# Optimization experiments

Measured on AMD Instinct MI355X. Metric: run time of the kernel, lower is better.

The kernel has to match this reference:

```python
import jax, jax.numpy as jnp
import numpy as np
import math

DIM = 4096
N_HEADS = 32
HEAD_DIM = DIM // N_HEADS  # 128
SEQLEN = 2048


def setup_inputs() -> dict:
    key = jax.random.key(0)
    ks = jax.random.split(key, 8)
    x = jax.random.normal(ks[0], (1, SEQLEN, DIM), dtype=jnp.float32)
    # freqs_cis as real view: (seqlen, head_dim//2, 2) = (cos, sin) of rotary angles
    theta = 10000.0 ** (-jnp.arange(0, HEAD_DIM, 2, dtype=jnp.float32) / HEAD_DIM)
    angles = jnp.arange(SEQLEN, dtype=jnp.float32)[:, None] * theta[None, :]
    freqs = jnp.stack([jnp.cos(angles), jnp.sin(angles)], axis=-1)  # (S, 64, 2)
    # causal additive mask (use -1e9 instead of -inf for numeric safety)
    mask = jnp.triu(jnp.full((SEQLEN, SEQLEN), -1e9, dtype=jnp.float32), k=1)[None, None]
    scale = 1.0 / math.sqrt(DIM)
    wq = jax.random.normal(ks[1], (DIM, DIM), dtype=jnp.float32) * scale
    wk = jax.random.normal(ks[2], (DIM, DIM), dtype=jnp.float32) * scale
    wv = jax.random.normal(ks[3], (DIM, DIM), dtype=jnp.float32) * scale
    wo = jax.random.normal(ks[4], (DIM, DIM), dtype=jnp.float32) * scale
    return {"x": x, "start_pos": 0, "freqs": freqs, "mask": mask,
            "wq": wq, "wk": wk, "wv": wv, "wo": wo}


def _rotary(xq, xk, freqs, seqlen, n_heads, head_dim):
    # Faithful to source: note the repo's slice(0, 2) means xq_ == xq (no pair swap).
    ll = freqs[:, :, 0:1]  # (S, hd/2, 1) cos
    rr = freqs[:, :, 1:2]  # (S, hd/2, 1) sin
    fl = jnp.concatenate([ll, ll], axis=-1).reshape(seqlen, 1, head_dim)
    fr = jnp.concatenate([-rr, rr], axis=-1).reshape(seqlen, 1, head_dim)
    xq_ = xq.reshape(seqlen, n_heads, head_dim // 2, 2).reshape(seqlen, n_heads, head_dim)  # == xq
    xk_ = xk.reshape(seqlen, n_heads, head_dim // 2, 2).reshape(seqlen, n_heads, head_dim)  # == xk
    return xq * fl + xq_ * fr, xk * fl + xk_ * fr


def reference(x, start_pos, freqs, mask, wq, wk, wv, wo):
    bsz, seqlen, dim = x.shape  # bsz == 1 (source squeezes batch)
    xs = x[0]  # (S, D) -- HE encrypt/linear/decrypt roundtrip == plain linear
    xq = xs @ wq.T
    xk = xs @ wk.T
    xv = xs @ wv.T
    xq = xq.reshape(seqlen, N_HEADS, HEAD_DIM)
    xk = xk.reshape(seqlen, N_HEADS, HEAD_DIM)
    xv = xv.reshape(seqlen, N_HEADS, HEAD_DIM)
    xq, xk = _rotary(xq, xk, freqs, seqlen, N_HEADS, HEAD_DIM)
    # start_pos == 0 and zero-initialized cache => keys/values are just xk/xv
    q = jnp.transpose(xq, (1, 0, 2))  # (H, S, Dh)
    k = jnp.transpose(xk, (1, 0, 2))
    v = jnp.transpose(xv, (1, 0, 2))
    scores = jnp.einsum('hqd,hkd->hqk', q, k) / math.sqrt(HEAD_DIM)  # (H, S, S)
    scores = scores[None] + mask  # (1, H, S, S)
    probs = jax.nn.softmax(scores, axis=-1)
    out = jnp.einsum('bhqk,hkd->bhqd', probs, v)  # (1, H, S, Dh)
    out = jnp.transpose(out, (0, 2, 1, 3)).reshape(bsz, seqlen, dim)
    return out @ wo.T
```

## Files before the change

kernel.cpp:

```cpp
#include <hip/hip_runtime.h>

#define DIM 4096
#define SEQ 2048
#define NH 32
#define HD 128

typedef __bf16 bf16x8 __attribute__((ext_vector_type(8)));
typedef float f32x4 __attribute__((ext_vector_type(4)));

#define QSCALE 0.12751649736765598f

__device__ inline ushort f2bf(float f) {
    union { float f; unsigned u; } v; v.f = f;
    unsigned r = v.u + 0x7fffu + ((v.u >> 16) & 1u);
    return (ushort)(r >> 16);
}

__global__ void conv_all(const float* __restrict__ x,  const float* __restrict__ wq,
                         const float* __restrict__ wk, const float* __restrict__ wv,
                         const float* __restrict__ wo,
                         ushort* __restrict__ xb,  ushort* __restrict__ wqb,
                         ushort* __restrict__ wkb, ushort* __restrict__ wvb,
                         ushort* __restrict__ wob) {
    int i = blockIdx.x * 256 + threadIdx.x;
    const float* src; ushort* dst; int off;
    const int n4x = (SEQ * DIM) / 4;
    if (i < n4x) { src = x; dst = xb; off = i; }
    else {
        int j = i - n4x;
        int w = j >> 22;
        off = j & ((1 << 22) - 1);
        src = (w == 0) ? wq : (w == 1) ? wk : (w == 2) ? wv : wo;
        dst = (w == 0) ? wqb : (w == 1) ? wkb : (w == 2) ? wvb : wob;
    }
    float4 v = ((const float4*)src)[off];
    ushort4 o;
    o.x = f2bf(v.x); o.y = f2bf(v.y); o.z = f2bf(v.z); o.w = f2bf(v.w);
    ((ushort4*)dst)[off] = o;
}


#define AS1(p) (const __attribute__((address_space(1))) void*)(p)
#define AS3(p) (__attribute__((address_space(3))) void*)(p)
#define FENCE() asm volatile("" ::: "memory")
#define BARRIER() do { FENCE(); __builtin_amdgcn_sched_barrier(0); \
    __builtin_amdgcn_s_barrier(); \
    __builtin_amdgcn_sched_barrier(0); FENCE(); } while (0)
#define LGKM0() do { asm volatile("s_waitcnt lgkmcnt(0)" ::: "memory"); \
    __builtin_amdgcn_sched_barrier(0); } while (0)

__device__ __forceinline__ void gemm256_body(
    const ushort* __restrict__ Ab,
    const ushort* __restrict__ Bb,
    ushort* __restrict__ sA0, ushort* __restrict__ sA1,
    ushort* __restrict__ sB0, ushort* __restrict__ sB1,
    f32x4 acc[8][4], const int K)
{
    const int tid  = threadIdx.x;
    const int wave = tid >> 6, lane = tid & 63;
    const int quad = lane >> 4, c = lane & 15;
    const int wm = wave >> 2, wn = wave & 3;

    const int aoff = (lane >> 3) * K + (((lane & 7) ^ (lane >> 3)) * 8);
    const int sa_r0 = wave * 8;
    const int sb_r0 = (wave >> 1) * 64 + (wave & 1) * 16;

    const int rp0 = ((0 * 4 + quad) ^ (c & 7)) * 8;
    const int rp1 = ((1 * 4 + quad) ^ (c & 7)) * 8;
    const int arow = (wm * 128 + c) * 64;
    const int brow = (wn * 64 + c) * 64;

#define STAGE_A(dst, h, k0) do { \
    const int _r0 = (h) * 64 + sa_r0; \
    __builtin_amdgcn_global_load_lds(AS1(Ab + (size_t)_r0 * K + (k0) + aoff), \
                                     AS3((dst) + _r0 * 64), 16, 0, 0); \
    const int _r1 = _r0 + 128; \
    __builtin_amdgcn_global_load_lds(AS1(Ab + (size_t)_r1 * K + (k0) + aoff), \
                                     AS3((dst) + _r1 * 64), 16, 0, 0); \
  } while (0)
#define STAGE_B(dst, h, k0) do { \
    const int _r0 = (h) * 32 + sb_r0; \
    __builtin_amdgcn_global_load_lds(AS1(Bb + (size_t)_r0 * K + (k0) + aoff), \
                                     AS3((dst) + _r0 * 64), 16, 0, 0); \
    const int _r1 = _r0 + 8; \
    __builtin_amdgcn_global_load_lds(AS1(Bb + (size_t)_r1 * K + (k0) + aoff), \
                                     AS3((dst) + _r1 * 64), 16, 0, 0); \
  } while (0)

    bf16x8 af[4][2], bfr[2][2];

#define READ_AH(buf, mh) do { \
    _Pragma("unroll") \
    for (int mt = 0; mt < 4; ++mt) { \
        af[mt][0] = *(const bf16x8*)&(buf)[arow + (mh) * 4096 + mt * 1024 + rp0]; \
        af[mt][1] = *(const bf16x8*)&(buf)[arow + (mh) * 4096 + mt * 1024 + rp1]; \
    } } while (0)
#define READ_BH(buf, nh) do { \
    _Pragma("unroll") \
    for (int nt = 0; nt < 2; ++nt) { \
        bfr[nt][0] = *(const bf16x8*)&(buf)[brow + (nh) * 2048 + nt * 1024 + rp0]; \
        bfr[nt][1] = *(const bf16x8*)&(buf)[brow + (nh) * 2048 + nt * 1024 + rp1]; \
    } } while (0)
#define MMA_Q(mh, nh) do { \
    __builtin_amdgcn_s_setprio(1); \
    _Pragma("unroll") \
    for (int kk = 0; kk < 2; ++kk) \
    _Pragma("unroll") \
    for (int mt = 0; mt < 4; ++mt) \
    _Pragma("unroll") \
    for (int nt = 0; nt < 2; ++nt) \
        acc[(mh)*4+mt][(nh)*2+nt] = __builtin_amdgcn_mfma_f32_16x16x32_bf16( \
            af[mt][kk], bfr[nt][kk], acc[(mh)*4+mt][(nh)*2+nt], 0, 0, 0); \
    __builtin_amdgcn_s_setprio(0); \
  } while (0)

    const int NT = K >> 6;

    STAGE_A(sA0, 0, 0);  STAGE_B(sB0, 0, 0);
    STAGE_A(sA0, 1, 0);  STAGE_B(sB0, 1, 0);
    STAGE_A(sA1, 0, 64); STAGE_B(sB1, 0, 64);
    asm volatile("s_waitcnt vmcnt(4)" ::: "memory");
    BARRIER();

    for (int t = 0; t < NT; ++t) {
        ushort* cA = (t & 1) ? sA1 : sA0;
        ushort* cB = (t & 1) ? sB1 : sB0;
        ushort* nA = (t & 1) ? sA0 : sA1;
        ushort* nB = (t & 1) ? sB0 : sB1;
        const int kn  = (t + 1) << 6;
        const int kn2 = (t + 2) << 6;
        const bool ok1 = (t + 1 < NT), ok2 = (t + 2 < NT);

        READ_AH(cA, 0); READ_BH(cB, 0);
        if (ok1) STAGE_A(nA, 1, kn);
        BARRIER(); LGKM0();
        MMA_Q(0, 0);
        BARRIER();

        READ_BH(cB, 1);
        if (ok1) STAGE_B(nB, 1, kn);
        BARRIER(); LGKM0();
        MMA_Q(0, 1);
        BARRIER();

        READ_AH(cA, 1); READ_BH(cB, 0);
        if (ok2) STAGE_A(cA, 0, kn2);
        BARRIER(); LGKM0();
        MMA_Q(1, 0);
        BARRIER();

        READ_BH(cB, 1);
        if (ok2) STAGE_B(cB, 0, kn2);
        BARRIER(); LGKM0();
        MMA_Q(1, 1);
        if (t < NT - 1) {
            if (ok2) asm volatile("s_waitcnt vmcnt(4)" ::: "memory");
            else     asm volatile("s_waitcnt vmcnt(0)" ::: "memory");
        }
        BARRIER();
    }
#undef STAGE_A
#undef STAGE_B
#undef READ_AH
#undef READ_BH
#undef MMA_Q
}

__global__ __launch_bounds__(512, 2)
void gemm_qkv(const ushort* __restrict__ A,
              const ushort* __restrict__ Bq, const ushort* __restrict__ Bk,
              const ushort* __restrict__ Bv,
              ushort* __restrict__ qout, ushort* __restrict__ kout,
              ushort* __restrict__ vt, const float* __restrict__ freqs) {
    __shared__ __align__(16) ushort sA[2][256 * 64];
    __shared__ __align__(16) ushort sB[2][256 * 64];
    const int bi = blockIdx.x;
    const int x = bi & 7;
    const int l = bi >> 3;
    const int mblk = l & 7;
    const int nblk = x * 6 + (l >> 3);
    const int wsel = nblk >> 4;
    const int nloc = (nblk & 15) * 256;
    const int m0 = mblk * 256;
    const ushort* B = (wsel == 0) ? Bq : (wsel == 1) ? Bk : Bv;

    const f32x4 vzero = {0.f, 0.f, 0.f, 0.f};
    f32x4 acc[8][4];
#pragma unroll
    for (int i = 0; i < 8; i++)
#pragma unroll
        for (int j = 0; j < 4; j++) acc[i][j] = vzero;

    gemm256_body(A + (size_t)m0 * DIM, B + (size_t)nloc * DIM,
                 &sA[0][0], &sA[1][0], &sB[0][0], &sB[1][0], acc, DIM);

    const int tid = threadIdx.x;
    const int wave = tid >> 6, lane = tid & 63;
    const int quad = lane >> 4, c = lane & 15;
    const int wm = wave >> 2, wn = wave & 3;

    if (wsel < 2) {
        ushort* Cw = wsel ? kout : qout;
        const float qs = wsel ? 1.0f : QSCALE;
#pragma unroll
        for (int i = 0; i < 8; i++) {
#pragma unroll
            for (int j = 0; j < 4; j++) {
                int colg = nloc + wn * 64 + j * 16 + c;
                int dh = (colg & 127) >> 1;
#pragma unroll
                for (int r = 0; r < 4; r++) {
                    int row = m0 + wm * 128 + i * 16 + quad * 4 + r;
                    float2 f2 = ((const float2*)freqs)[row * 64 + dh];
                    float f = (f2.x + ((c & 1) ? f2.y : -f2.y)) * qs;
                    Cw[(size_t)row * DIM + colg] = f2bf(acc[i][j][r] * f);
                }
            }
        }
    } else {
#pragma unroll
        for (int i = 0; i < 8; i++) {
#pragma unroll
            for (int j = 0; j < 4; j++) {
                int cv = nloc + wn * 64 + j * 16 + c;
                int row0 = m0 + wm * 128 + i * 16 + quad * 4;
                ushort4 o;
                o.x = f2bf(acc[i][j][0]); o.y = f2bf(acc[i][j][1]);
                o.z = f2bf(acc[i][j][2]); o.w = f2bf(acc[i][j][3]);
                *(ushort4*)&vt[(size_t)cv * SEQ + row0] = o;
            }
        }
    }
}

__global__ __launch_bounds__(512, 2)
void gemm_f32out(const ushort* __restrict__ A, const ushort* __restrict__ B,
                 float* __restrict__ C, int M, int N, int K) {
    __shared__ __align__(16) ushort sA[2][256 * 64];
    __shared__ __align__(16) ushort sB[2][256 * 64];
    const int bi = blockIdx.x;
    const int x = bi & 7;
    const int l = bi >> 3;
    const int mblk = l & 7;
    const int nblk = x * 2 + (l >> 3);
    const int m0 = mblk * 256, n0 = nblk * 256;

    const f32x4 vzero = {0.f, 0.f, 0.f, 0.f};
    f32x4 acc[8][4];
#pragma unroll
    for (int i = 0; i < 8; i++)
#pragma unroll
        for (int j = 0; j < 4; j++) acc[i][j] = vzero;

    gemm256_body(A + (size_t)m0 * K, B + (size_t)n0 * K,
                 &sA[0][0], &sA[1][0], &sB[0][0], &sB[1][0], acc, K);

    const int tid = threadIdx.x;
    const int wave = tid >> 6, lane = tid & 63;
    const int quad = lane >> 4, c = lane & 15;
    const int wm = wave >> 2, wn = wave & 3;

#pragma unroll
    for (int i = 0; i < 8; i++)
#pragma unroll
        for (int j = 0; j < 4; j++)
#pragma unroll
            for (int r = 0; r < 4; r++) {
                int row = m0 + wm * 128 + i * 16 + quad * 4 + r;
                int col = n0 + wn * 64 + j * 16 + c;
                C[(size_t)row * N + col] = acc[i][j][r];
            }
}

__global__ __launch_bounds__(256)
void flash_kernel(const ushort* __restrict__ Q, const ushort* __restrict__ K,
                  const ushort* __restrict__ Vt, ushort* __restrict__ O) {
    const int bi = blockIdx.x;
    const int h = bi & (NH - 1);
    const int p = bi >> 5;
    __shared__ __align__(16) ushort sK[64 * 128];
    __shared__ __align__(16) ushort sVt[128 * 64];
    __shared__ __align__(16) ushort sP[4][16 * 72];
    const int tid = threadIdx.x, wave = tid >> 6, lane = tid & 63;
    const int quad = lane >> 4, c = lane & 15;

    for (int pass = 0; pass < 2; pass++) {
        const int qb = pass ? (SEQ / 64 - 1 - p) : p;
        const int q0 = qb * 64;

        bf16x8 qf[4];
        {
            const ushort* Qp = Q + (size_t)(q0 + wave * 16 + c) * DIM + h * HD;
#pragma unroll
            for (int ks = 0; ks < 4; ks++) qf[ks] = *(const bf16x8*)(Qp + ks * 32 + quad * 8);
        }
        const f32x4 vzero = {0.f, 0.f, 0.f, 0.f};
        f32x4 oa[8];
#pragma unroll
        for (int dt = 0; dt < 8; dt++) oa[dt] = vzero;
        float ms[4], ls[4];
#pragma unroll
        for (int r = 0; r < 4; r++) { ms[r] = -1e30f; ls[r] = 0.f; }

        for (int kt = 0; kt <= qb; kt++) {
            __syncthreads();
#pragma unroll
            for (int i = 0; i < 4; i++) {
                int lr = wave * 16 + i * 4 + (lane >> 4);
                int ch = lane & 15;
                int g = (ch & 8) | ((ch ^ lr) & 7);
                __builtin_amdgcn_global_load_lds(
                    (const __attribute__((address_space(1))) void*)(K + (size_t)(kt * 64 + lr) * DIM + h * HD + g * 8),
                    (__attribute__((address_space(3))) void*)(&sK[(wave * 16 + i * 4) * 128]), 16, 0, 0);
            }
#pragma unroll
            for (int i = 0; i < 4; i++) {
                int ld = wave * 32 + i * 8 + (lane >> 3);
                int ch = lane & 7;
                int g = (ch ^ ld) & 7;
                __builtin_amdgcn_global_load_lds(
                    (const __attribute__((address_space(1))) void*)(Vt + (size_t)(h * HD + ld) * SEQ + kt * 64 + g * 8),
                    (__attribute__((address_space(3))) void*)(&sVt[(wave * 32 + i * 8) * 64]), 16, 0, 0);
            }
            __syncthreads();

            f32x4 s[4];
#pragma unroll
            for (int nt = 0; nt < 4; nt++) s[nt] = vzero;
#pragma unroll
            for (int ks = 0; ks < 4; ks++)
#pragma unroll
                for (int nt = 0; nt < 4; nt++) {
                    int lr = nt * 16 + c;
                    int gc = ks * 4 + quad;
                    int pch = (gc & 8) | ((gc ^ lr) & 7);
                    bf16x8 kf = *(const bf16x8*)&sK[lr * 128 + pch * 8];
                    s[nt] = __builtin_amdgcn_mfma_f32_16x16x32_bf16(qf[ks], kf, s[nt], 0, 0, 0);
                }

            if (kt == qb) {
#pragma unroll
                for (int nt = 0; nt < 4; nt++)
#pragma unroll
                    for (int r = 0; r < 4; r++) {
                        int keyg = nt * 16 + c;
                        int qg   = wave * 16 + quad * 4 + r;
                        if (keyg > qg) s[nt][r] = -1e30f;
                    }
            }

            float mnew[4], alpha[4];
#pragma unroll
            for (int r = 0; r < 4; r++) {
                float v = fmaxf(fmaxf(s[0][r], s[1][r]), fmaxf(s[2][r], s[3][r]));
                v = fmaxf(v, __shfl_xor(v, 1));
                v = fmaxf(v, __shfl_xor(v, 2));
                v = fmaxf(v, __shfl_xor(v, 4));
                v = fmaxf(v, __shfl_xor(v, 8));
                mnew[r]  = fmaxf(ms[r], v);
                alpha[r] = exp2f(ms[r] - mnew[r]);
                ms[r]    = mnew[r];
            }
            float rs[4] = {0.f, 0.f, 0.f, 0.f};
#pragma unroll
            for (int nt = 0; nt < 4; nt++)
#pragma unroll
                for (int r = 0; r < 4; r++) {
                    float pv = exp2f(s[nt][r] - mnew[r]);
                    rs[r] += pv;
                    sP[wave][(quad * 4 + r) * 72 + nt * 16 + c] = f2bf(pv);
                }
#pragma unroll
            for (int r = 0; r < 4; r++) {
                float v = rs[r];
                v += __shfl_xor(v, 1);
                v += __shfl_xor(v, 2);
                v += __shfl_xor(v, 4);
                v += __shfl_xor(v, 8);
                ls[r] = ls[r] * alpha[r] + v;
            }
#pragma unroll
            for (int dt = 0; dt < 8; dt++)
#pragma unroll
                for (int r = 0; r < 4; r++) oa[dt][r] *= alpha[r];

            __asm__ volatile("s_waitcnt lgkmcnt(0)" ::: "memory");

#pragma unroll
            for (int k2 = 0; k2 < 2; k2++) {
                bf16x8 pf = *(const bf16x8*)&sP[wave][c * 72 + k2 * 32 + quad * 8];
#pragma unroll
                for (int dt = 0; dt < 8; dt++) {
                    int ld = dt * 16 + c;
                    int gc = k2 * 4 + quad;
                    int pch = (gc ^ ld) & 7;
                    bf16x8 vf = *(const bf16x8*)&sVt[ld * 64 + pch * 8];
                    oa[dt] = __builtin_amdgcn_mfma_f32_16x16x32_bf16(pf, vf, oa[dt], 0, 0, 0);
                }
            }
        }

#pragma unroll
        for (int r = 0; r < 4; r++) {
            float inv = 1.f / ls[r];
            int row = q0 + wave * 16 + quad * 4 + r;
#pragma unroll
            for (int dt = 0; dt < 8; dt++)
                O[(size_t)row * DIM + h * HD + dt * 16 + c] = f2bf(oa[dt][r] * inv);
        }
    }
}

extern "C" void kernel_launch(void* const* d_in, const int* in_sizes, int n_in,
                              void* d_out, int out_size, void* d_ws, size_t ws_size,
                              hipStream_t stream) {
    const float* x     = (const float*)d_in[0];
    const float* freqs = (const float*)d_in[2];
    const float* wq    = (const float*)d_in[4];
    const float* wk    = (const float*)d_in[5];
    const float* wv    = (const float*)d_in[6];
    const float* wo    = (const float*)d_in[7];
    float* out = (float*)d_out;

    ushort* xb    = (ushort*)d_ws;
    ushort* wqb   = xb    + (size_t)SEQ * DIM;
    ushort* wkb   = wqb   + (size_t)DIM * DIM;
    ushort* wvb   = wkb   + (size_t)DIM * DIM;
    ushort* wob   = wvb   + (size_t)DIM * DIM;
    ushort* qbuf  = wob   + (size_t)DIM * DIM;
    ushort* kbuf  = qbuf  + (size_t)SEQ * DIM;
    ushort* vtbuf = kbuf  + (size_t)SEQ * DIM;
    ushort* obuf  = vtbuf + (size_t)SEQ * DIM;

    const int n4tot = (SEQ * DIM + 4 * DIM * DIM) / 4;
    conv_all<<<n4tot / 256, 256, 0, stream>>>(x, wq, wk, wv, wo, xb, wqb, wkb, wvb, wob);

    gemm_qkv<<<dim3(384), 512, 0, stream>>>(xb, wqb, wkb, wvb, qbuf, kbuf, vtbuf, freqs);

    flash_kernel<<<dim3(NH * SEQ / 128), 256, 0, stream>>>(qbuf, kbuf, vtbuf, obuf);

    gemm_f32out<<<dim3(128), 512, 0, stream>>>(obuf, wob, out, SEQ, DIM, DIM);
}
```

Before: 749.0 us.

## Shrink GEMM tiles to 128x256 to double block count and simplify pipeline

Both bf16 GEMMs move from 256x256 to 128x256 output tiles, which doubles the grid (768 and 256 blocks) so the 256 CUs get better occupancy and wave balance. The K-loop is restructured from four quarter-steps to two half-steps: all B fragments are read once, the B tile is staged in one go, and the explicit lgkmcnt waits and sched_barriers are dropped. The tradeoff is lower arithmetic intensity per block, meaning more global and LDS traffic per FLOP, and possibly weaker scheduling control now that the sched barriers are gone.

Measured after the change: 751.0 us. Within noise of the previous version (+0.3%).

```diff
diff --git a/kernel.cpp b/kernel.cpp
--- a/kernel.cpp
+++ b/kernel.cpp
@@ -43,18 +43,14 @@
 #define AS1(p) (const __attribute__((address_space(1))) void*)(p)
 #define AS3(p) (__attribute__((address_space(3))) void*)(p)
 #define FENCE() asm volatile("" ::: "memory")
-#define BARRIER() do { FENCE(); __builtin_amdgcn_sched_barrier(0); \
-    __builtin_amdgcn_s_barrier(); \
-    __builtin_amdgcn_sched_barrier(0); FENCE(); } while (0)
-#define LGKM0() do { asm volatile("s_waitcnt lgkmcnt(0)" ::: "memory"); \
-    __builtin_amdgcn_sched_barrier(0); } while (0)
-
-__device__ __forceinline__ void gemm256_body(
+#define BARRIER() do { FENCE(); __builtin_amdgcn_s_barrier(); FENCE(); } while (0)
+
+__device__ __forceinline__ void gemm128x256_body(
     const ushort* __restrict__ Ab,
     const ushort* __restrict__ Bb,
     ushort* __restrict__ sA0, ushort* __restrict__ sA1,
     ushort* __restrict__ sB0, ushort* __restrict__ sB1,
-    f32x4 acc[8][4], const int K)
+    f32x4 acc[4][4], const int K)
 {
     const int tid  = threadIdx.x;
     const int wave = tid >> 6, lane = tid & 63;
@@ -62,108 +58,91 @@
     const int wm = wave >> 2, wn = wave & 3;
 
     const int aoff = (lane >> 3) * K + (((lane & 7) ^ (lane >> 3)) * 8);
-    const int sa_r0 = wave * 8;
-    const int sb_r0 = (wave >> 1) * 64 + (wave & 1) * 16;
+    const int ra0 = (wave >> 2) * 64 + (wave & 3) * 8;
+    const int rb0 = wave * 8;
 
     const int rp0 = ((0 * 4 + quad) ^ (c & 7)) * 8;
     const int rp1 = ((1 * 4 + quad) ^ (c & 7)) * 8;
-    const int arow = (wm * 128 + c) * 64;
+    const int arow = (wm * 64 + c) * 64;
     const int brow = (wn * 64 + c) * 64;
 
 #define STAGE_A(dst, h, k0) do { \
-    const int _r0 = (h) * 64 + sa_r0; \
-    __builtin_amdgcn_global_load_lds(AS1(Ab + (size_t)_r0 * K + (k0) + aoff), \
-                                     AS3((dst) + _r0 * 64), 16, 0, 0); \
-    const int _r1 = _r0 + 128; \
-    __builtin_amdgcn_global_load_lds(AS1(Ab + (size_t)_r1 * K + (k0) + aoff), \
-                                     AS3((dst) + _r1 * 64), 16, 0, 0); \
+    const int _r = ra0 + (h) * 32; \
+    __builtin_amdgcn_global_load_lds(AS1(Ab + (size_t)_r * K + (k0) + aoff), \
+                                     AS3((dst) + _r * 64), 16, 0, 0); \
   } while (0)
-#define STAGE_B(dst, h, k0) do { \
-    const int _r0 = (h) * 32 + sb_r0; \
-    __builtin_amdgcn_global_load_lds(AS1(Bb + (size_t)_r0 * K + (k0) + aoff), \
-                                     AS3((dst) + _r0 * 64), 16, 0, 0); \
-    const int _r1 = _r0 + 8; \
-    __builtin_amdgcn_global_load_lds(AS1(Bb + (size_t)_r1 * K + (k0) + aoff), \
-                                     AS3((dst) + _r1 * 64), 16, 0, 0); \
-  } while (0)
-
-    bf16x8 af[4][2], bfr[2][2];
-
-#define READ_AH(buf, mh) do { \
-    _Pragma("unroll") \
-    for (int mt = 0; mt < 4; ++mt) { \
-        af[mt][0] = *(const bf16x8*)&(buf)[arow + (mh) * 4096 + mt * 1024 + rp0]; \
-        af[mt][1] = *(const bf16x8*)&(buf)[arow + (mh) * 4096 + mt * 1024 + rp1]; \
+#define STAGE_B4(dst, k0) do { \
+    _Pragma("unroll") \
+    for (int _q = 0; _q < 4; ++_q) { \
+        const int _r = rb0 + _q * 64; \
+        __builtin_amdgcn_global_load_lds(AS1(Bb + (size_t)_r * K + (k0) + aoff), \
+                                         AS3((dst) + _r * 64), 16, 0, 0); \
     } } while (0)
-#define READ_BH(buf, nh) do { \
-    _Pragma("unroll") \
-    for (int nt = 0; nt < 2; ++nt) { \
-        bfr[nt][0] = *(const bf16x8*)&(buf)[brow + (nh) * 2048 + nt * 1024 + rp0]; \
-        bfr[nt][1] = *(const bf16x8*)&(buf)[brow + (nh) * 2048 + nt * 1024 + rp1]; \
+
+    bf16x8 af[2][2], bfr[4][2];
+
+#define READ_AH(buf, h) do { \
+    _Pragma("unroll") \
+    for (int _i = 0; _i < 2; ++_i) { \
+        af[_i][0] = *(const bf16x8*)&(buf)[arow + ((h) * 2 + _i) * 1024 + rp0]; \
+        af[_i][1] = *(const bf16x8*)&(buf)[arow + ((h) * 2 + _i) * 1024 + rp1]; \
     } } while (0)
-#define MMA_Q(mh, nh) do { \
+#define READ_BALL(buf) do { \
+    _Pragma("unroll") \
+    for (int _n = 0; _n < 4; ++_n) { \
+        bfr[_n][0] = *(const bf16x8*)&(buf)[brow + _n * 1024 + rp0]; \
+        bfr[_n][1] = *(const bf16x8*)&(buf)[brow + _n * 1024 + rp1]; \
+    } } while (0)
+#define MMA_H(h) do { \
     __builtin_amdgcn_s_setprio(1); \
     _Pragma("unroll") \
-    for (int kk = 0; kk < 2; ++kk) \
-    _Pragma("unroll") \
-    for (int mt = 0; mt < 4; ++mt) \
-    _Pragma("unroll") \
-    for (int nt = 0; nt < 2; ++nt) \
-        acc[(mh)*4+mt][(nh)*2+nt] = __builtin_amdgcn_mfma_f32_16x16x32_bf16( \
-            af[mt][kk], bfr[nt][kk], acc[(mh)*4+mt][(nh)*2+nt], 0, 0, 0); \
+    for (int _kk = 0; _kk < 2; ++_kk) \
+    _Pragma("unroll") \
+    for (int _i = 0; _i < 2; ++_i) \
+    _Pragma("unroll") \
+    for (int _n = 0; _n < 4; ++_n) \
+        acc[(h) * 2 + _i][_n] = __builtin_amdgcn_mfma_f32_16x16x32_bf16( \
+            af[_i][_kk], bfr[_n][_kk], acc[(h) * 2 + _i][_n], 0, 0, 0); \
     __builtin_amdgcn_s_setprio(0); \
   } while (0)
 
     const int NT = K >> 6;
 
-    STAGE_A(sA0, 0, 0);  STAGE_B(sB0, 0, 0);
-    STAGE_A(sA0, 1, 0);  STAGE_B(sB0, 1, 0);
-    STAGE_A(sA1, 0, 64); STAGE_B(sB1, 0, 64);
-    asm volatile("s_waitcnt vmcnt(4)" ::: "memory");
+    STAGE_A(sA0, 0, 0); STAGE_A(sA0, 1, 0); STAGE_B4(sB0, 0);
+    STAGE_A(sA1, 0, 64); STAGE_B4(sB1, 64);
+    asm volatile("s_waitcnt vmcnt(5)" ::: "memory");
     BARRIER();
 
+#pragma unroll 1
     for (int t = 0; t < NT; ++t) {
         ushort* cA = (t & 1) ? sA1 : sA0;
         ushort* cB = (t & 1) ? sB1 : sB0;
         ushort* nA = (t & 1) ? sA0 : sA1;
-        ushort* nB = (t & 1) ? sB0 : sB1;
         const int kn  = (t + 1) << 6;
         const int kn2 = (t + 2) << 6;
         const bool ok1 = (t + 1 < NT), ok2 = (t + 2 < NT);
 
-        READ_AH(cA, 0); READ_BH(cB, 0);
+        READ_AH(cA, 0); READ_BALL(cB);
         if (ok1) STAGE_A(nA, 1, kn);
-        BARRIER(); LGKM0();
-        MMA_Q(0, 0);
         BARRIER();
-
-        READ_BH(cB, 1);
-        if (ok1) STAGE_B(nB, 1, kn);
-        BARRIER(); LGKM0();
-        MMA_Q(0, 1);
+        MMA_H(0);
         BARRIER();
 
-        READ_AH(cA, 1); READ_BH(cB, 0);
-        if (ok2) STAGE_A(cA, 0, kn2);
-        BARRIER(); LGKM0();
-        MMA_Q(1, 0);
+        READ_AH(cA, 1);
+        if (ok2) { STAGE_A(cA, 0, kn2); STAGE_B4(cB, kn2); }
         BARRIER();
-
-        READ_BH(cB, 1);
-        if (ok2) STAGE_B(cB, 0, kn2);
-        BARRIER(); LGKM0();
-        MMA_Q(1, 1);
+        MMA_H(1);
         if (t < NT - 1) {
-            if (ok2) asm volatile("s_waitcnt vmcnt(4)" ::: "memory");
+            if (ok2) asm volatile("s_waitcnt vmcnt(5)" ::: "memory");
             else     asm volatile("s_waitcnt vmcnt(0)" ::: "memory");
         }
         BARRIER();
     }
 #undef STAGE_A
-#undef STAGE_B
+#undef STAGE_B4
 #undef READ_AH
-#undef READ_BH
-#undef MMA_Q
+#undef READ_BALL
+#undef MMA_H
 }
 
 __global__ __launch_bounds__(512, 2)
@@ -172,27 +151,27 @@
               const ushort* __restrict__ Bv,
               ushort* __restrict__ qout, ushort* __restrict__ kout,
               ushort* __restrict__ vt, const float* __restrict__ freqs) {
-    __shared__ __align__(16) ushort sA[2][256 * 64];
+    __shared__ __align__(16) ushort sA[2][128 * 64];
     __shared__ __align__(16) ushort sB[2][256 * 64];
     const int bi = blockIdx.x;
     const int x = bi & 7;
     const int l = bi >> 3;
-    const int mblk = l & 7;
-    const int nblk = x * 6 + (l >> 3);
+    const int mblk = l & 15;
+    const int nblk = x * 6 + (l >> 4);
     const int wsel = nblk >> 4;
     const int nloc = (nblk & 15) * 256;
-    const int m0 = mblk * 256;
+    const int m0 = mblk * 128;
     const ushort* B = (wsel == 0) ? Bq : (wsel == 1) ? Bk : Bv;
 
     const f32x4 vzero = {0.f, 0.f, 0.f, 0.f};
-    f32x4 acc[8][4];
-#pragma unroll
-    for (int i = 0; i < 8; i++)
+    f32x4 acc[4][4];
+#pragma unroll
+    for (int i = 0; i < 4; i++)
 #pragma unroll
         for (int j = 0; j < 4; j++) acc[i][j] = vzero;
 
-    gemm256_body(A + (size_t)m0 * DIM, B + (size_t)nloc * DIM,
-                 &sA[0][0], &sA[1][0], &sB[0][0], &sB[1][0], acc, DIM);
+    gemm128x256_body(A + (size_t)m0 * DIM, B + (size_t)nloc * DIM,
+                     &sA[0][0], &sA[1][0], &sB[0][0], &sB[1][0], acc, DIM);
 
     const int tid = threadIdx.x;
     const int wave = tid >> 6, lane = tid & 63;
@@ -203,30 +182,30 @@
         ushort* Cw = wsel ? kout : qout;
         const float qs = wsel ? 1.0f : QSCALE;
 #pragma unroll
-        for (int i = 0; i < 8; i++) {
-#pragma unroll
-            for (int j = 0; j < 4; j++) {
-                int colg = nloc + wn * 64 + j * 16 + c;
+        for (int mt = 0; mt < 4; mt++) {
+#pragma unroll
+            for (int nt = 0; nt < 4; nt++) {
+                int colg = nloc + wn * 64 + nt * 16 + c;
                 int dh = (colg & 127) >> 1;
 #pragma unroll
                 for (int r = 0; r < 4; r++) {
-                    int row = m0 + wm * 128 + i * 16 + quad * 4 + r;
+                    int row = m0 + wm * 64 + mt * 16 + quad * 4 + r;
                     float2 f2 = ((const float2*)freqs)[row * 64 + dh];
                     float f = (f2.x + ((c & 1) ? f2.y : -f2.y)) * qs;
-                    Cw[(size_t)row * DIM + colg] = f2bf(acc[i][j][r] * f);
+                    Cw[(size_t)row * DIM + colg] = f2bf(acc[mt][nt][r] * f);
                 }
             }
         }
     } else {
 #pragma unroll
-        for (int i = 0; i < 8; i++) {
-#pragma unroll
-            for (int j = 0; j < 4; j++) {
-                int cv = nloc + wn * 64 + j * 16 + c;
-                int row0 = m0 + wm * 128 + i * 16 + quad * 4;
+        for (int mt = 0; mt < 4; mt++) {
+#pragma unroll
+            for (int nt = 0; nt < 4; nt++) {
+                int cv = nloc + wn * 64 + nt * 16 + c;
+                int row0 = m0 + wm * 64 + mt * 16 + quad * 4;
                 ushort4 o;
-                o.x = f2bf(acc[i][j][0]); o.y = f2bf(acc[i][j][1]);
-                o.z = f2bf(acc[i][j][2]); o.w = f2bf(acc[i][j][3]);
+                o.x = f2bf(acc[mt][nt][0]); o.y = f2bf(acc[mt][nt][1]);
+                o.z = f2bf(acc[mt][nt][2]); o.w = f2bf(acc[mt][nt][3]);
                 *(ushort4*)&vt[(size_t)cv * SEQ + row0] = o;
             }
         }
@@ -236,24 +215,24 @@
 __global__ __launch_bounds__(512, 2)
 void gemm_f32out(const ushort* __restrict__ A, const ushort* __restrict__ B,
                  float* __restrict__ C, int M, int N, int K) {
-    __shared__ __align__(16) ushort sA[2][256 * 64];
+    __shared__ __align__(16) ushort sA[2][128 * 64];
     __shared__ __align__(16) ushort sB[2][256 * 64];
     const int bi = blockIdx.x;
     const int x = bi & 7;
     const int l = bi >> 3;
-    const int mblk = l & 7;
-    const int nblk = x * 2 + (l >> 3);
-    const int m0 = mblk * 256, n0 = nblk * 256;
+    const int mblk = l & 15;
+    const int nblk = x * 2 + (l >> 4);
+    const int m0 = mblk * 128, n0 = nblk * 256;
 
     const f32x4 vzero = {0.f, 0.f, 0.f, 0.f};
-    f32x4 acc[8][4];
-#pragma unroll
-    for (int i = 0; i < 8; i++)
+    f32x4 acc[4][4];
+#pragma unroll
+    for (int i = 0; i < 4; i++)
 #pragma unroll
         for (int j = 0; j < 4; j++) acc[i][j] = vzero;
 
-    gemm256_body(A + (size_t)m0 * K, B + (size_t)n0 * K,
-                 &sA[0][0], &sA[1][0], &sB[0][0], &sB[1][0], acc, K);
+    gemm128x256_body(A + (size_t)m0 * K, B + (size_t)n0 * K,
+                     &sA[0][0], &sA[1][0], &sB[0][0], &sB[1][0], acc, K);
 
     const int tid = threadIdx.x;
     const int wave = tid >> 6, lane = tid & 63;
@@ -261,14 +240,14 @@
     const int wm = wave >> 2, wn = wave & 3;
 
 #pragma unroll
-    for (int i = 0; i < 8; i++)
-#pragma unroll
-        for (int j = 0; j < 4; j++)
+    for (int mt = 0; mt < 4; mt++)
+#pragma unroll
+        for (int nt = 0; nt < 4; nt++)
 #pragma unroll
             for (int r = 0; r < 4; r++) {
-                int row = m0 + wm * 128 + i * 16 + quad * 4 + r;
-                int col = n0 + wn * 64 + j * 16 + c;
-                C[(size_t)row * N + col] = acc[i][j][r];
+                int row = m0 + wm * 64 + mt * 16 + quad * 4 + r;
+                int col = n0 + wn * 64 + nt * 16 + c;
+                C[(size_t)row * N + col] = acc[mt][nt][r];
             }
 }
 
@@ -435,9 +414,9 @@
     const int n4tot = (SEQ * DIM + 4 * DIM * DIM) / 4;
     conv_all<<<n4tot / 256, 256, 0, stream>>>(x, wq, wk, wv, wo, xb, wqb, wkb, wvb, wob);
 
-    gemm_qkv<<<dim3(384), 512, 0, stream>>>(xb, wqb, wkb, wvb, qbuf, kbuf, vtbuf, freqs);
+    gemm_qkv<<<dim3(768), 512, 0, stream>>>(xb, wqb, wkb, wvb, qbuf, kbuf, vtbuf, freqs);
 
     flash_kernel<<<dim3(NH * SEQ / 128), 256, 0, stream>>>(qbuf, kbuf, vtbuf, obuf);
 
-    gemm_f32out<<<dim3(128), 512, 0, stream>>>(obuf, wob, out, SEQ, DIM, DIM);
-}
+    gemm_f32out<<<dim3(256), 512, 0, stream>>>(obuf, wob, out, SEQ, DIM, DIM);
+}
```

## Restructure GEMM pipeline to keep all B fragments and prefetch two tiles ahead

Applied to the files above, without the earlier changes.

The shared 256x256 GEMM mainloop now holds all four B fragments in registers, so B is read from LDS once per k-tile instead of twice. Global-to-LDS staging is reorganised to fill both buffers fully up front and then refill the current buffer for tile t+2 across the four sub-phases, waiting on vmcnt(8). The explicit lgkmcnt(0) waits and sched_barriers are removed, leaving the compiler to insert LDS waits, and the loop is marked unroll 1. The aim is less LDS read traffic and deeper prefetch, at the cost of more VGPRs and more loads in flight. Overwriting the current buffer while other waves may still be reading it depends on the barrier placement being correct.

New measurement: 759.3 us. No clear change (+1.4%).

```diff
diff --git a/kernel.cpp b/kernel.cpp
--- a/kernel.cpp
+++ b/kernel.cpp
@@ -43,11 +43,7 @@
 #define AS1(p) (const __attribute__((address_space(1))) void*)(p)
 #define AS3(p) (__attribute__((address_space(3))) void*)(p)
 #define FENCE() asm volatile("" ::: "memory")
-#define BARRIER() do { FENCE(); __builtin_amdgcn_sched_barrier(0); \
-    __builtin_amdgcn_s_barrier(); \
-    __builtin_amdgcn_sched_barrier(0); FENCE(); } while (0)
-#define LGKM0() do { asm volatile("s_waitcnt lgkmcnt(0)" ::: "memory"); \
-    __builtin_amdgcn_sched_barrier(0); } while (0)
+#define BARRIER() do { FENCE(); __builtin_amdgcn_s_barrier(); FENCE(); } while (0)
 
 __device__ __forceinline__ void gemm256_body(
     const ushort* __restrict__ Ab,
@@ -61,12 +57,12 @@
     const int quad = lane >> 4, c = lane & 15;
     const int wm = wave >> 2, wn = wave & 3;
 
-    const int aoff = (lane >> 3) * K + (((lane & 7) ^ (lane >> 3)) * 8);
+    const int aoff  = (lane >> 3) * K + (((lane & 7) ^ (lane >> 3)) * 8);
     const int sa_r0 = wave * 8;
     const int sb_r0 = (wave >> 1) * 64 + (wave & 1) * 16;
 
-    const int rp0 = ((0 * 4 + quad) ^ (c & 7)) * 8;
-    const int rp1 = ((1 * 4 + quad) ^ (c & 7)) * 8;
+    const int rp0 = (quad ^ (c & 7)) * 8;
+    const int rp1 = ((4 + quad) ^ (c & 7)) * 8;
     const int arow = (wm * 128 + c) * 64;
     const int brow = (wn * 64 + c) * 64;
 
@@ -87,82 +83,79 @@
                                      AS3((dst) + _r1 * 64), 16, 0, 0); \
   } while (0)
 
-    bf16x8 af[4][2], bfr[2][2];
-
-#define READ_AH(buf, mh) do { \
+    bf16x8 af[4][2], bfr[4][2];
+
+#define READ_A(buf, mh) do { \
     _Pragma("unroll") \
-    for (int mt = 0; mt < 4; ++mt) { \
-        af[mt][0] = *(const bf16x8*)&(buf)[arow + (mh) * 4096 + mt * 1024 + rp0]; \
-        af[mt][1] = *(const bf16x8*)&(buf)[arow + (mh) * 4096 + mt * 1024 + rp1]; \
+    for (int _m = 0; _m < 4; ++_m) { \
+        af[_m][0] = *(const bf16x8*)&(buf)[arow + (mh) * 4096 + _m * 1024 + rp0]; \
+        af[_m][1] = *(const bf16x8*)&(buf)[arow + (mh) * 4096 + _m * 1024 + rp1]; \
     } } while (0)
-#define READ_BH(buf, nh) do { \
+#define READ_B2(buf, nh) do { \
     _Pragma("unroll") \
-    for (int nt = 0; nt < 2; ++nt) { \
-        bfr[nt][0] = *(const bf16x8*)&(buf)[brow + (nh) * 2048 + nt * 1024 + rp0]; \
-        bfr[nt][1] = *(const bf16x8*)&(buf)[brow + (nh) * 2048 + nt * 1024 + rp1]; \
+    for (int _n = 0; _n < 2; ++_n) { \
+        bfr[(nh) * 2 + _n][0] = *(const bf16x8*)&(buf)[brow + (nh) * 2048 + _n * 1024 + rp0]; \
+        bfr[(nh) * 2 + _n][1] = *(const bf16x8*)&(buf)[brow + (nh) * 2048 + _n * 1024 + rp1]; \
     } } while (0)
-#define MMA_Q(mh, nh) do { \
+#define MMA_Q(mh, nq) do { \
     __builtin_amdgcn_s_setprio(1); \
     _Pragma("unroll") \
-    for (int kk = 0; kk < 2; ++kk) \
+    for (int _kk = 0; _kk < 2; ++_kk) \
     _Pragma("unroll") \
-    for (int mt = 0; mt < 4; ++mt) \
+    for (int _m = 0; _m < 4; ++_m) \
     _Pragma("unroll") \
-    for (int nt = 0; nt < 2; ++nt) \
-        acc[(mh)*4+mt][(nh)*2+nt] = __builtin_amdgcn_mfma_f32_16x16x32_bf16( \
-            af[mt][kk], bfr[nt][kk], acc[(mh)*4+mt][(nh)*2+nt], 0, 0, 0); \
+    for (int _n = 0; _n < 2; ++_n) \
+        acc[(mh) * 4 + _m][(nq) * 2 + _n] = __builtin_amdgcn_mfma_f32_16x16x32_bf16( \
+            af[_m][_kk], bfr[(nq) * 2 + _n][_kk], acc[(mh) * 4 + _m][(nq) * 2 + _n], 0, 0, 0); \
     __builtin_amdgcn_s_setprio(0); \
   } while (0)
 
     const int NT = K >> 6;
 
-    STAGE_A(sA0, 0, 0);  STAGE_B(sB0, 0, 0);
-    STAGE_A(sA0, 1, 0);  STAGE_B(sB0, 1, 0);
-    STAGE_A(sA1, 0, 64); STAGE_B(sB1, 0, 64);
-    asm volatile("s_waitcnt vmcnt(4)" ::: "memory");
+    STAGE_A(sA0, 0, 0);  STAGE_A(sA0, 1, 0);
+    STAGE_B(sB0, 0, 0);  STAGE_B(sB0, 1, 0);
+    STAGE_A(sA1, 0, 64); STAGE_A(sA1, 1, 64);
+    STAGE_B(sB1, 0, 64); STAGE_B(sB1, 1, 64);
+    asm volatile("s_waitcnt vmcnt(8)" ::: "memory");
     BARRIER();
 
+#pragma unroll 1
     for (int t = 0; t < NT; ++t) {
         ushort* cA = (t & 1) ? sA1 : sA0;
         ushort* cB = (t & 1) ? sB1 : sB0;
-        ushort* nA = (t & 1) ? sA0 : sA1;
-        ushort* nB = (t & 1) ? sB0 : sB1;
-        const int kn  = (t + 1) << 6;
         const int kn2 = (t + 2) << 6;
-        const bool ok1 = (t + 1 < NT), ok2 = (t + 2 < NT);
-
-        READ_AH(cA, 0); READ_BH(cB, 0);
-        if (ok1) STAGE_A(nA, 1, kn);
-        BARRIER(); LGKM0();
+        const bool ok2 = (t + 2 < NT);
+
+        READ_A(cA, 0); READ_B2(cB, 0);
+        BARRIER();
         MMA_Q(0, 0);
         BARRIER();
 
-        READ_BH(cB, 1);
-        if (ok1) STAGE_B(nB, 1, kn);
-        BARRIER(); LGKM0();
+        READ_B2(cB, 1);
+        if (ok2) { STAGE_A(cA, 0, kn2); STAGE_B(cB, 0, kn2); }
+        BARRIER();
         MMA_Q(0, 1);
         BARRIER();
 
-        READ_AH(cA, 1); READ_BH(cB, 0);
-        if (ok2) STAGE_A(cA, 0, kn2);
-        BARRIER(); LGKM0();
+        READ_A(cA, 1);
+        if (ok2) STAGE_B(cB, 1, kn2);
+        BARRIER();
         MMA_Q(1, 0);
         BARRIER();
 
-        READ_BH(cB, 1);
-        if (ok2) STAGE_B(cB, 0, kn2);
-        BARRIER(); LGKM0();
+        if (ok2) STAGE_A(cA, 1, kn2);
+        BARRIER();
         MMA_Q(1, 1);
         if (t < NT - 1) {
-            if (ok2) asm volatile("s_waitcnt vmcnt(4)" ::: "memory");
+            if (ok2) asm volatile("s_waitcnt vmcnt(8)" ::: "memory");
             else     asm volatile("s_waitcnt vmcnt(0)" ::: "memory");
         }
         BARRIER();
     }
 #undef STAGE_A
 #undef STAGE_B
-#undef READ_AH
-#undef READ_BH
+#undef READ_A
+#undef READ_B2
 #undef MMA_Q
 }
 
```
